# Optimization experiments

Hardware: AMD Instinct MI355X
Metric: run time of the kernel (lower is better)

## Reference

```python
import jax, jax.numpy as jnp
import numpy as np

B, N, T, D, H = 4, 8, 512, 256, 8
DK = D // H


def _dwconv(x, w, b=None):
    # x: (BN, D, T) depthwise conv, kernel 3, padding 'same', groups=D
    y = jax.lax.conv_general_dilated(
        x, w, window_strides=(1,), padding='SAME',
        feature_group_count=x.shape[1],
        dimension_numbers=('NCH', 'OIH', 'NCH'))
    if b is not None:
        y = y + b[None, :, None]
    return y


def setup_inputs() -> dict:
    key = jax.random.key(0)
    ks = jax.random.split(key, 16)
    s = 1.0 / np.sqrt(D)
    s3 = 1.0 / np.sqrt(3 * D)
    inp = {
        'query': jax.random.normal(ks[0], (B, N, T, D), jnp.float32),
        'key': jax.random.normal(ks[1], (B, N, T, D), jnp.float32),
        'value': jax.random.normal(ks[2], (B, N, T, D), jnp.float32),
        'key_padding_mask': jax.random.randint(ks[3], (B, N, T), 0, 2, jnp.int32),
        # depthwise conv params
        'w_pos': jax.random.uniform(ks[4], (D, 1, 3), jnp.float32, -0.577, 0.577),
        'b_pos': jax.random.uniform(ks[5], (D,), jnp.float32, -0.577, 0.577),
        # physics-initialized differential operators (still learnable floats)
        'w_vel': jnp.tile(jnp.array([-1.0, 0.0, 1.0], jnp.float32)[None, None, :], (D, 1, 1)),
        'w_acc': jnp.tile(jnp.array([1.0, -2.0, 1.0], jnp.float32)[None, None, :], (D, 1, 1)),
        # fusion / projection linears (stored as (in, out))
        'Wq': jax.random.uniform(ks[6], (3 * D, D), jnp.float32, -s3, s3),
        'bq': jax.random.uniform(ks[7], (D,), jnp.float32, -s3, s3),
        'Wk': jax.random.uniform(ks[8], (3 * D, D), jnp.float32, -s3, s3),
        'bk': jax.random.uniform(ks[9], (D,), jnp.float32, -s3, s3),
        'Wv': jax.random.uniform(ks[10], (D, D), jnp.float32, -s, s),
        'bv': jax.random.uniform(ks[11], (D,), jnp.float32, -s, s),
        'Wo': jax.random.uniform(ks[12], (D, D), jnp.float32, -s, s),
        'bo': jax.random.uniform(ks[13], (D,), jnp.float32, -s, s),
    }
    return inp


def reference(query, key, value, key_padding_mask,
              w_pos, b_pos, w_vel, w_acc,
              Wq, bq, Wk, bk, Wv, bv, Wo, bo):
    b, n, t, d = query.shape
    scale = jnp.float32(1.0 / np.sqrt(DK))

    def kin_feats(x):
        xin = x.reshape(b * n, t, d).transpose(0, 2, 1)  # (BN, D, T)
        p = _dwconv(xin, w_pos, b_pos)
        v = _dwconv(xin, w_vel)
        a = _dwconv(xin, w_acc)
        return jnp.concatenate([p, v, a], axis=1).transpose(0, 2, 1)  # (BN, T, 3D)

    qc = kin_feats(query)
    kc = kin_feats(key)

    Q = (qc @ Wq + bq).reshape(b, n, t, H, DK).transpose(0, 1, 3, 2, 4)  # (B,N,H,Tq,dk)
    K = (kc @ Wk + bk).reshape(b, n, t, H, DK).transpose(0, 1, 3, 2, 4)
    V = (value @ Wv + bv).reshape(b, n, t, H, DK).transpose(0, 1, 3, 2, 4)

    scores = jnp.einsum('bnhqd,bnhkd->bnhqk', Q, K) * scale
    mask = key_padding_mask.astype(bool)[:, :, None, None, :]  # (B,N,1,1,Tk)
    scores = jnp.where(mask, jnp.float32(-1e9), scores)
    attn = jax.nn.softmax(scores, axis=-1)  # dropout is identity in eval

    ctx = jnp.einsum('bnhqk,bnhkd->bnhqd', attn, V)
    ctx = ctx.transpose(0, 1, 3, 2, 4).reshape(b, n, t, d)
    return ctx @ Wo + bo
```

## Files before the change

kernel.cpp:

```cpp
#include <hip/hip_runtime.h>
#include <math.h>


typedef __attribute__((ext_vector_type(8))) short bf16x8;
typedef __attribute__((ext_vector_type(4))) float f32x4;
typedef __attribute__((ext_vector_type(4))) int i32x4;

__device__ __forceinline__ unsigned short f2bf(float f) {
    unsigned u = __float_as_uint(f);
    return (unsigned short)((u + 0x7fff + ((u >> 16) & 1)) >> 16);
}
__device__ __forceinline__ float bf2f(unsigned short h) {
    return __uint_as_float(((unsigned)h) << 16);
}
__device__ __forceinline__ float ex2(float x) {
    float r; asm("v_exp_f32 %0, %1" : "=v"(r) : "v"(x)); return r;
}
__device__ __forceinline__ int cvtpk(float lo, float hi) {
    int r; asm("v_cvt_pk_bf16_f32 %0, %1, %2" : "=v"(r) : "v"(lo), "v"(hi)); return r;
}
__device__ __forceinline__ void gll16(const void* gsrc, const void* ldst) {
    __builtin_amdgcn_global_load_lds(
        (const __attribute__((address_space(1))) unsigned int*)gsrc,
        (__attribute__((address_space(3))) unsigned int*)ldst, 16, 0, 0);
}

#define SCL (0.17677669529663689f * 1.4426950408889634f)

#define OFF_XPQ  0u
#define OFF_XPK  8421376u
#define OFF_VB   16842752u
#define OFF_BTQ  25231360u
#define OFF_BTK  25624576u
#define OFF_BEFF 26017792u
#define OFF_WVT  26019840u
#define OFF_WOT  26150912u
#define OFF_QB   26413056u
#define OFF_KB   34801664u
#define OFF_VV   43190272u
#define OFF_CTX  51578880u

__global__ __launch_bounds__(256) void cvtprep(
    const float* __restrict__ q, const float* __restrict__ k, const float* __restrict__ v,
    unsigned short* __restrict__ xpq, unsigned short* __restrict__ xpk,
    unsigned short* __restrict__ vb,
    const float* __restrict__ Wq, const float* __restrict__ Wk,
    const float* __restrict__ bq, const float* __restrict__ bk,
    const float* __restrict__ wp, const float* __restrict__ wv,
    const float* __restrict__ wa, const float* __restrict__ b_pos,
    const float* __restrict__ Wv, const float* __restrict__ Wo,
    unsigned short* __restrict__ BtQ, unsigned short* __restrict__ BtK,
    float* __restrict__ beff, unsigned short* __restrict__ WVT,
    unsigned short* __restrict__ WOT)
{
    int bid = blockIdx.x;
    if (bid < 4112) {
        int idx = bid * 256 + threadIdx.x;
        int which = idx / 526336;
        int r = idx - which * 526336;
        int bn = r / 16448;
        int rr = r - bn * 16448;
        int p = rr >> 5;
        int c8 = (rr & 31) * 8;
        const float* src = which ? k : q;
        unsigned short* dst = which ? xpk : xpq;
        unsigned o[4] = {0, 0, 0, 0};
        if (p != 0 && p != 513) {
            const float* s = src + ((size_t)(bn * 512 + p - 1) * 256 + c8);
            float4 a = *(const float4*)s;
            float4 b = *(const float4*)(s + 4);
            o[0] = f2bf(a.x) | ((unsigned)f2bf(a.y) << 16);
            o[1] = f2bf(a.z) | ((unsigned)f2bf(a.w) << 16);
            o[2] = f2bf(b.x) | ((unsigned)f2bf(b.y) << 16);
            o[3] = f2bf(b.z) | ((unsigned)f2bf(b.w) << 16);
        }
        unsigned* d = (unsigned*)(dst + ((size_t)(bn * 514 + p) * 256 + c8));
        d[0] = o[0]; d[1] = o[1]; d[2] = o[2]; d[3] = o[3];
    } else if (bid < 6160) {
        int idx = (bid - 4112) * 256 + threadIdx.x;
        int row = idx >> 5;
        int c8 = (idx & 31) * 8;
        const float* s = v + ((size_t)row * 256 + c8);
        float4 a = *(const float4*)s;
        float4 b = *(const float4*)(s + 4);
        unsigned* d = (unsigned*)(vb + ((size_t)row * 256 + c8));
        d[0] = f2bf(a.x) | ((unsigned)f2bf(a.y) << 16);
        d[1] = f2bf(a.z) | ((unsigned)f2bf(a.w) << 16);
        d[2] = f2bf(b.x) | ((unsigned)f2bf(b.y) << 16);
        d[3] = f2bf(b.z) | ((unsigned)f2bf(b.w) << 16);
    } else if (bid < 7696) {
        int idx = (bid - 6160) * 256 + threadIdx.x;
        int which = idx / 196608;
        int r = idx - which * 196608;
        int j = r >> 16;
        int rem = r & 65535;
        int n = rem >> 8;
        int d = rem & 255;
        const float* W = which ? Wk : Wq;
        float val = wp[d * 3 + j] * W[d * 256 + n]
                  + wv[d * 3 + j] * W[(256 + d) * 256 + n]
                  + wa[d * 3 + j] * W[(512 + d) * 256 + n];
        if (!which) val *= SCL;
        (which ? BtK : BtQ)[n * 768 + j * 256 + d] = f2bf(val);
    } else if (bid < 8208) {
        int idx = (bid - 7696) * 256 + threadIdx.x;
        int which = idx >> 16;
        int r = idx & 65535;
        int n = r >> 8, kk = r & 255;
        if (!which) {
            WVT[n * 256 + kk] = f2bf(Wv[kk * 256 + n]);
        } else {
            float vv = Wo[kk * 256 + n];
            unsigned short hi = f2bf(vv);
            WOT[n * 512 + kk] = hi;
            WOT[n * 512 + 256 + kk] = f2bf(vv - bf2f(hi));
        }
    } else {
        int which = bid - 8208;
        int n = threadIdx.x;
        const float* W = which ? Wk : Wq;
        const float* bb = which ? bk : bq;
        float s = bb[n];
        for (int d = 0; d < 256; ++d) s = fmaf(b_pos[d], W[d * 256 + n], s);
        if (!which) s *= SCL;
        beff[which * 256 + n] = s;
    }
}

template<typename OutT>
__device__ __forceinline__ void gemm_body(
    const unsigned short* __restrict__ A, const unsigned short* __restrict__ Bt,
    const float* __restrict__ bias, OutT* __restrict__ Out,
    int ktot, int btstride, int im2col,
    unsigned short* As, unsigned short* Bs)
{
    const int tid = threadIdx.x;
    const int wid = tid >> 6, l = tid & 63;
    const int g = l >> 4, r15 = l & 15;
    const int wm = wid & 1, wn = wid >> 1;
    const int m0 = blockIdx.x * 64, n0 = blockIdx.y * 128;

    f32x4 acc[2][4] = {};

    auto stage = [&](int k0, int b) {
        unsigned short* as = As + b * 4096;
        unsigned short* bs = Bs + b * 8192;
        #pragma unroll
        for (int qq = 0; qq < 2; ++qq) {
            int cidx = qq * 256 + wid * 64 + l;
            int row = cidx >> 3, csrc = ((cidx & 7) ^ (row & 7)) * 8;
            const unsigned short* src;
            if (im2col) {
                int seq = m0 >> 9, t0 = m0 & 511, j = k0 >> 8, c0 = k0 & 255;
                src = A + ((size_t)(seq * 514 + t0 + row + j) * 256 + c0 + csrc);
            } else {
                src = A + ((size_t)(m0 + row) * 256 + (k0 & 255) + csrc);
            }
            gll16(src, as + qq * 2048 + wid * 512);
        }
        #pragma unroll
        for (int qq = 0; qq < 4; ++qq) {
            int cidx = qq * 256 + wid * 64 + l;
            int row = cidx >> 3, csrc = ((cidx & 7) ^ (row & 7)) * 8;
            gll16(Bt + ((size_t)(n0 + row) * btstride + k0 + csrc), bs + qq * 2048 + wid * 512);
        }
    };

    stage(0, 0);
    __syncthreads();
    int b = 0;
    for (int k0 = 0; k0 < ktot; k0 += 64, b ^= 1) {
        if (k0 + 64 < ktot) stage(k0 + 64, b ^ 1);
        const unsigned short* as = As + b * 4096;
        const unsigned short* bs = Bs + b * 8192;
        #pragma unroll
        for (int s = 0; s < 2; ++s) {
            const int ch = ((s * 4 + g) ^ (r15 & 7)) * 8;
            bf16x8 af[2], bf[4];
            #pragma unroll
            for (int mt = 0; mt < 2; ++mt)
                af[mt] = *(const bf16x8*)&as[(wm * 32 + mt * 16 + r15) * 64 + ch];
            #pragma unroll
            for (int nt = 0; nt < 4; ++nt)
                bf[nt] = *(const bf16x8*)&bs[(wn * 64 + nt * 16 + r15) * 64 + ch];
            #pragma unroll
            for (int mt = 0; mt < 2; ++mt)
                #pragma unroll
                for (int nt = 0; nt < 4; ++nt)
                    acc[mt][nt] = __builtin_amdgcn_mfma_f32_16x16x32_bf16(af[mt], bf[nt], acc[mt][nt], 0, 0, 0);
        }
        __syncthreads();
    }

    #pragma unroll
    for (int nt = 0; nt < 4; ++nt) {
        const int col = n0 + wn * 64 + nt * 16 + r15;
        const float bb = bias[col];
        #pragma unroll
        for (int mt = 0; mt < 2; ++mt)
            #pragma unroll
            for (int r = 0; r < 4; ++r) {
                const size_t row = m0 + wm * 32 + mt * 16 + 4 * g + r;
                float vv = acc[mt][nt][r] + bb;
                if constexpr (sizeof(OutT) == 2) Out[row * 256 + col] = (OutT)f2bf(vv);
                else Out[row * 256 + col] = (OutT)vv;
            }
    }
}

__global__ __launch_bounds__(256) void proj_fused(
    const unsigned short* __restrict__ XPQ, const unsigned short* __restrict__ XPK,
    const unsigned short* __restrict__ VB,
    const unsigned short* __restrict__ BTQ, const unsigned short* __restrict__ BTK,
    const unsigned short* __restrict__ WVT,
    const float* __restrict__ BEFF, const float* __restrict__ bv,
    unsigned short* __restrict__ QB, unsigned short* __restrict__ KB,
    unsigned short* __restrict__ VV)
{
    __shared__ alignas(16) unsigned short As[2 * 4096];
    __shared__ alignas(16) unsigned short Bs[2 * 8192];
    const int z = blockIdx.z;
    const unsigned short* A  = z == 0 ? XPQ : (z == 1 ? XPK : VB);
    const unsigned short* Bt = z == 0 ? BTQ : (z == 1 ? BTK : WVT);
    const float* bias        = z == 0 ? BEFF : (z == 1 ? BEFF + 256 : bv);
    unsigned short* Out      = z == 0 ? QB : (z == 1 ? KB : VV);
    const int ktot = z < 2 ? 768 : 256;
    gemm_body<unsigned short>(A, Bt, bias, Out, ktot, ktot, z < 2 ? 1 : 0, As, Bs);
}

__global__ __launch_bounds__(256) void outproj(
    const unsigned short* __restrict__ CTX, const unsigned short* __restrict__ WOT,
    const float* __restrict__ bo, float* __restrict__ Out)
{
    __shared__ alignas(16) unsigned short As[2 * 4096];
    __shared__ alignas(16) unsigned short Bs[2 * 8192];
    gemm_body<float>(CTX, WOT, bo, Out, 512, 512, 0, As, Bs);
}

__global__ __launch_bounds__(256) void attn_mfma(const unsigned short* __restrict__ Qb,
                                                 const unsigned short* __restrict__ Kb,
                                                 const unsigned short* __restrict__ Vv,
                                                 const int* __restrict__ mask,
                                                 unsigned short* __restrict__ ctx) {
    __shared__ alignas(16) unsigned short Qs[64 * 32];
    __shared__ alignas(16) unsigned short Ks[2][128 * 32];
    __shared__ alignas(16) unsigned short VsT[2][32 * 136];
    __shared__ float Mb[2][128];

    const int qt = blockIdx.x, bnh = blockIdx.y;
    const int bn = bnh >> 3, h = bnh & 7;
    const int tid = threadIdx.x, wid = tid >> 6, l = tid & 63;
    const int g = l >> 4, r15 = l & 15;
    const unsigned short* Qg = Qb + (size_t)bn * 512 * 256 + h * 32;
    const unsigned short* Kg = Kb + (size_t)bn * 512 * 256 + h * 32;
    const unsigned short* Vg = Vv + (size_t)bn * 512 * 256 + h * 32;
    const int* mp = mask + bn * 512;

    auto stageK = [&](int k0, int b) {
        #pragma unroll
        for (int qq = 0; qq < 2; ++qq) {
            int cidx = qq * 256 + wid * 64 + l;
            int row = cidx >> 2, csrc = ((cidx & 3) ^ (row & 3)) * 8;
            gll16(Kg + ((size_t)(k0 + row)) * 256 + csrc, &Ks[b][qq * 2048 + wid * 512]);
        }
    };

    {
        int cidx = wid * 64 + l;
        gll16(Qg + ((size_t)(qt * 64 + (cidx >> 2))) * 256 + (cidx & 3) * 8, Qs + wid * 512);
    }
    stageK(0, 0);
    {
        #pragma unroll
        for (int qq = 0; qq < 2; ++qq) {
            int key = l + 64 * qq;
            i32x4 vr = *(const i32x4*)(const void*)(Vg + (size_t)key * 256 + wid * 8);
            #pragma unroll
            for (int i = 0; i < 4; ++i) {
                unsigned u = (unsigned)vr[i];
                VsT[0][(wid * 8 + 2 * i) * 136 + key] = (unsigned short)(u & 0xffff);
                VsT[0][(wid * 8 + 2 * i + 1) * 136 + key] = (unsigned short)(u >> 16);
            }
        }
        if (tid < 128) Mb[0][tid] = (mp[tid] != 0) ? -1e9f : 0.f;
    }
    __syncthreads();

    const bf16x8 bq = *(const bf16x8*)&Qs[(wid * 16 + r15) * 32 + g * 8];

    float mrun = -1e30f, lrun = 0.f;
    f32x4 accO[2] = {};

    for (int kt = 0; kt < 4; ++kt) {
        const int cur = kt & 1, nxt = cur ^ 1;
        const int k0n = kt * 128 + 128;

        i32x4 vr[2];
        int mraw = 0;
        if (kt < 3) {
            stageK(k0n, nxt);
            #pragma unroll
            for (int qq = 0; qq < 2; ++qq)
                vr[qq] = *(const i32x4*)(const void*)(Vg + ((size_t)(k0n + l + 64 * qq)) * 256 + wid * 8);
            if (tid < 128) mraw = mp[k0n + tid];
        }

        float p[8][4];
        float rmax = -3e38f;
        __builtin_amdgcn_s_setprio(1);
        #pragma unroll
        for (int t2 = 0; t2 < 8; ++t2) {
            const int base = 32 * (t2 >> 1) + 4 * (t2 & 1);
            const int arow = base + 8 * (r15 >> 2) + (r15 & 3);
            bf16x8 ak = *(const bf16x8*)&Ks[cur][arow * 32 + ((g ^ (arow & 3)) * 8)];
            f32x4 cin = *(const f32x4*)&Mb[cur][base + 8 * g];
            f32x4 st = __builtin_amdgcn_mfma_f32_16x16x32_bf16(ak, bq, cin, 0, 0, 0);
            #pragma unroll
            for (int r = 0; r < 4; ++r) p[t2][r] = st[r];
            rmax = fmaxf(rmax, fmaxf(fmaxf(st[0], st[1]), fmaxf(st[2], st[3])));
        }
        __builtin_amdgcn_s_setprio(0);
        rmax = fmaxf(rmax, __shfl_xor(rmax, 16, 64));
        rmax = fmaxf(rmax, __shfl_xor(rmax, 32, 64));

        if (__ballot(rmax > mrun)) {
            float mnew = fmaxf(mrun, rmax);
            float fs = ex2(mrun - mnew);
            lrun *= fs;
            accO[0] *= fs;
            accO[1] *= fs;
            mrun = mnew;
        }
        float psum = 0.f;
        #pragma unroll
        for (int t2 = 0; t2 < 8; ++t2)
            #pragma unroll
            for (int r = 0; r < 4; ++r) {
                float e = ex2(p[t2][r] - mrun);
                p[t2][r] = e;
                psum += e;
            }
        psum += __shfl_xor(psum, 16, 64);
        psum += __shfl_xor(psum, 32, 64);
        lrun += psum;

        bf16x8 pb[4];
        #pragma unroll
        for (int s = 0; s < 4; ++s) {
            i32x4 bi = {cvtpk(p[2 * s][0], p[2 * s][1]), cvtpk(p[2 * s][2], p[2 * s][3]),
                        cvtpk(p[2 * s + 1][0], p[2 * s + 1][1]), cvtpk(p[2 * s + 1][2], p[2 * s + 1][3])};
            pb[s] = __builtin_bit_cast(bf16x8, bi);
        }

        __builtin_amdgcn_s_setprio(1);
        #pragma unroll
        for (int mt = 0; mt < 2; ++mt)
            #pragma unroll
            for (int s = 0; s < 4; ++s) {
                bf16x8 av = *(const bf16x8*)&VsT[cur][(mt * 16 + r15) * 136 + 32 * s + 8 * g];
                accO[mt] = __builtin_amdgcn_mfma_f32_16x16x32_bf16(av, pb[s], accO[mt], 0, 0, 0);
            }
        __builtin_amdgcn_s_setprio(0);

        if (kt < 3) {
            #pragma unroll
            for (int qq = 0; qq < 2; ++qq) {
                int key = l + 64 * qq;
                #pragma unroll
                for (int i = 0; i < 4; ++i) {
                    unsigned u = (unsigned)vr[qq][i];
                    VsT[nxt][(wid * 8 + 2 * i) * 136 + key] = (unsigned short)(u & 0xffff);
                    VsT[nxt][(wid * 8 + 2 * i + 1) * 136 + key] = (unsigned short)(u >> 16);
                }
            }
            if (tid < 128) Mb[nxt][tid] = (mraw != 0) ? -1e9f : 0.f;
        }
        __syncthreads();
    }

    const float inv = 1.f / lrun;
    const size_t orow = (size_t)bn * 512 + qt * 64 + wid * 16 + r15;
    #pragma unroll
    for (int mt = 0; mt < 2; ++mt) {
        ushort4 o;
        o.x = f2bf(accO[mt][0] * inv);
        o.y = f2bf(accO[mt][1] * inv);
        o.z = f2bf(accO[mt][2] * inv);
        o.w = f2bf(accO[mt][3] * inv);
        *(ushort4*)&ctx[orow * 256 + h * 32 + mt * 16 + 4 * g] = o;
    }
}

extern "C" void kernel_launch(void* const* d_in, const int* in_sizes, int n_in,
                              void* d_out, int out_size, void* d_ws, size_t ws_size,
                              hipStream_t stream) {
    const float* query = (const float*)d_in[0];
    const float* key   = (const float*)d_in[1];
    const float* value = (const float*)d_in[2];
    const int*   kpm   = (const int*)d_in[3];
    const float* w_pos = (const float*)d_in[4];
    const float* b_pos = (const float*)d_in[5];
    const float* w_vel = (const float*)d_in[6];
    const float* w_acc = (const float*)d_in[7];
    const float* Wq    = (const float*)d_in[8];
    const float* bq    = (const float*)d_in[9];
    const float* Wk    = (const float*)d_in[10];
    const float* bk    = (const float*)d_in[11];
    const float* Wv    = (const float*)d_in[12];
    const float* bv    = (const float*)d_in[13];
    const float* Wo    = (const float*)d_in[14];
    const float* bo    = (const float*)d_in[15];

    unsigned char* w = (unsigned char*)d_ws;
    unsigned short* XPQ = (unsigned short*)(w + OFF_XPQ);
    unsigned short* XPK = (unsigned short*)(w + OFF_XPK);
    unsigned short* VB  = (unsigned short*)(w + OFF_VB);
    unsigned short* BTQ = (unsigned short*)(w + OFF_BTQ);
    unsigned short* BTK = (unsigned short*)(w + OFF_BTK);
    float*          BEFF= (float*)(w + OFF_BEFF);
    unsigned short* WVT = (unsigned short*)(w + OFF_WVT);
    unsigned short* WOT = (unsigned short*)(w + OFF_WOT);
    unsigned short* QB  = (unsigned short*)(w + OFF_QB);
    unsigned short* KB  = (unsigned short*)(w + OFF_KB);
    unsigned short* VV  = (unsigned short*)(w + OFF_VV);
    unsigned short* CTX = (unsigned short*)(w + OFF_CTX);

    cvtprep<<<8210, 256, 0, stream>>>(query, key, value, XPQ, XPK, VB,
                                      Wq, Wk, bq, bk, w_pos, w_vel, w_acc, b_pos,
                                      Wv, Wo, BTQ, BTK, BEFF, WVT, WOT);

    proj_fused<<<dim3(256, 2, 3), 256, 0, stream>>>(XPQ, XPK, VB, BTQ, BTK, WVT,
                                                    BEFF, bv, QB, KB, VV);

    attn_mfma<<<dim3(8, 256), 256, 0, stream>>>(QB, KB, VV, kpm, CTX);

    outproj<<<dim3(256, 2), 256, 0, stream>>>(CTX, WOT, bo, (float*)d_out);
}
```

Measured before the change: 96.66 us.

## Fuse fp32-to-bf16 input conversion into projection GEMM and use 32x32 MFMA tiles

Removes the separate pass that converted query/key/value to padded bf16 buffers. The projection GEMM now loads fp32 activations directly, handles the conv boundary padding with a validity check, and converts to bf16 in registers before writing to shared memory. The GEMM body also moves from 16x16x32 to 32x32x16 MFMA, with each block covering the full 256-wide N dimension, which halves the grid but doubles the B tile in LDS. The intent is to cut a full read and write of the activations through global memory. The cost is larger LDS use, which can lower occupancy, and fewer blocks.

```diff
diff --git a/kernel.cpp b/kernel.cpp
--- a/kernel.cpp
+++ b/kernel.cpp
@@ -4,6 +4,7 @@
 
 typedef __attribute__((ext_vector_type(8))) short bf16x8;
 typedef __attribute__((ext_vector_type(4))) float f32x4;
+typedef __attribute__((ext_vector_type(16))) float f32x16;
 typedef __attribute__((ext_vector_type(4))) int i32x4;
 
 __device__ __forceinline__ unsigned short f2bf(float f) {
@@ -27,9 +28,6 @@
 
 #define SCL (0.17677669529663689f * 1.4426950408889634f)
 
-#define OFF_XPQ  0u
-#define OFF_XPK  8421376u
-#define OFF_VB   16842752u
 #define OFF_BTQ  25231360u
 #define OFF_BTK  25624576u
 #define OFF_BEFF 26017792u
@@ -40,56 +38,24 @@
 #define OFF_VV   43190272u
 #define OFF_CTX  51578880u
 
-__global__ __launch_bounds__(256) void cvtprep(
-    const float* __restrict__ q, const float* __restrict__ k, const float* __restrict__ v,
-    unsigned short* __restrict__ xpq, unsigned short* __restrict__ xpk,
-    unsigned short* __restrict__ vb,
-    const float* __restrict__ Wq, const float* __restrict__ Wk,
-    const float* __restrict__ bq, const float* __restrict__ bk,
-    const float* __restrict__ wp, const float* __restrict__ wv,
-    const float* __restrict__ wa, const float* __restrict__ b_pos,
-    const float* __restrict__ Wv, const float* __restrict__ Wo,
-    unsigned short* __restrict__ BtQ, unsigned short* __restrict__ BtK,
-    float* __restrict__ beff, unsigned short* __restrict__ WVT,
-    unsigned short* __restrict__ WOT)
-{
+__global__ __launch_bounds__(256) void prep(const float* __restrict__ Wq,
+                                            const float* __restrict__ Wk,
+                                            const float* __restrict__ bq,
+                                            const float* __restrict__ bk,
+                                            const float* __restrict__ wp,
+                                            const float* __restrict__ wv,
+                                            const float* __restrict__ wa,
+                                            const float* __restrict__ b_pos,
+                                            const float* __restrict__ Wv,
+                                            const float* __restrict__ Wo,
+                                            unsigned short* __restrict__ BtQ,
+                                            unsigned short* __restrict__ BtK,
+                                            float* __restrict__ beff,
+                                            unsigned short* __restrict__ WVT,
+                                            unsigned short* __restrict__ WOT) {
     int bid = blockIdx.x;
-    if (bid < 4112) {
+    if (bid < 1536) {
         int idx = bid * 256 + threadIdx.x;
-        int which = idx / 526336;
-        int r = idx - which * 526336;
-        int bn = r / 16448;
-        int rr = r - bn * 16448;
-        int p = rr >> 5;
-        int c8 = (rr & 31) * 8;
-        const float* src = which ? k : q;
-        unsigned short* dst = which ? xpk : xpq;
-        unsigned o[4] = {0, 0, 0, 0};
-        if (p != 0 && p != 513) {
-            const float* s = src + ((size_t)(bn * 512 + p - 1) * 256 + c8);
-            float4 a = *(const float4*)s;
-            float4 b = *(const float4*)(s + 4);
-            o[0] = f2bf(a.x) | ((unsigned)f2bf(a.y) << 16);
-            o[1] = f2bf(a.z) | ((unsigned)f2bf(a.w) << 16);
-            o[2] = f2bf(b.x) | ((unsigned)f2bf(b.y) << 16);
-            o[3] = f2bf(b.z) | ((unsigned)f2bf(b.w) << 16);
-        }
-        unsigned* d = (unsigned*)(dst + ((size_t)(bn * 514 + p) * 256 + c8));
-        d[0] = o[0]; d[1] = o[1]; d[2] = o[2]; d[3] = o[3];
-    } else if (bid < 6160) {
-        int idx = (bid - 4112) * 256 + threadIdx.x;
-        int row = idx >> 5;
-        int c8 = (idx & 31) * 8;
-        const float* s = v + ((size_t)row * 256 + c8);
-        float4 a = *(const float4*)s;
-        float4 b = *(const float4*)(s + 4);
-        unsigned* d = (unsigned*)(vb + ((size_t)row * 256 + c8));
-        d[0] = f2bf(a.x) | ((unsigned)f2bf(a.y) << 16);
-        d[1] = f2bf(a.z) | ((unsigned)f2bf(a.w) << 16);
-        d[2] = f2bf(b.x) | ((unsigned)f2bf(b.y) << 16);
-        d[3] = f2bf(b.z) | ((unsigned)f2bf(b.w) << 16);
-    } else if (bid < 7696) {
-        int idx = (bid - 6160) * 256 + threadIdx.x;
         int which = idx / 196608;
         int r = idx - which * 196608;
         int j = r >> 16;
@@ -102,21 +68,21 @@
                   + wa[d * 3 + j] * W[(512 + d) * 256 + n];
         if (!which) val *= SCL;
         (which ? BtK : BtQ)[n * 768 + j * 256 + d] = f2bf(val);
-    } else if (bid < 8208) {
-        int idx = (bid - 7696) * 256 + threadIdx.x;
+    } else if (bid < 2048) {
+        int idx = (bid - 1536) * 256 + threadIdx.x;
         int which = idx >> 16;
         int r = idx & 65535;
-        int n = r >> 8, kk = r & 255;
+        int n = r >> 8, k = r & 255;
         if (!which) {
-            WVT[n * 256 + kk] = f2bf(Wv[kk * 256 + n]);
+            WVT[n * 256 + k] = f2bf(Wv[k * 256 + n]);
         } else {
-            float vv = Wo[kk * 256 + n];
-            unsigned short hi = f2bf(vv);
-            WOT[n * 512 + kk] = hi;
-            WOT[n * 512 + 256 + kk] = f2bf(vv - bf2f(hi));
+            float v = Wo[k * 256 + n];
+            unsigned short hi = f2bf(v);
+            WOT[n * 512 + k] = hi;
+            WOT[n * 512 + 256 + k] = f2bf(v - bf2f(hi));
         }
     } else {
-        int which = bid - 8208;
+        int which = bid - 2048;
         int n = threadIdx.x;
         const float* W = which ? Wk : Wq;
         const float* bb = which ? bk : bq;
@@ -127,90 +93,124 @@
     }
 }
 
-template<typename OutT>
-__device__ __forceinline__ void gemm_body(
-    const unsigned short* __restrict__ A, const unsigned short* __restrict__ Bt,
+template<int MODE, int KTOT, typename OutT>
+__device__ __forceinline__ void gemm32_body(
+    const void* Asrc, const unsigned short* __restrict__ Bt,
     const float* __restrict__ bias, OutT* __restrict__ Out,
-    int ktot, int btstride, int im2col,
     unsigned short* As, unsigned short* Bs)
 {
     const int tid = threadIdx.x;
     const int wid = tid >> 6, l = tid & 63;
-    const int g = l >> 4, r15 = l & 15;
-    const int wm = wid & 1, wn = wid >> 1;
-    const int m0 = blockIdx.x * 64, n0 = blockIdx.y * 128;
-
-    f32x4 acc[2][4] = {};
-
-    auto stage = [&](int k0, int b) {
-        unsigned short* as = As + b * 4096;
-        unsigned short* bs = Bs + b * 8192;
-        #pragma unroll
-        for (int qq = 0; qq < 2; ++qq) {
-            int cidx = qq * 256 + wid * 64 + l;
-            int row = cidx >> 3, csrc = ((cidx & 7) ^ (row & 7)) * 8;
-            const unsigned short* src;
-            if (im2col) {
-                int seq = m0 >> 9, t0 = m0 & 511, j = k0 >> 8, c0 = k0 & 255;
-                src = A + ((size_t)(seq * 514 + t0 + row + j) * 256 + c0 + csrc);
+    const int l31 = l & 31, h2 = l >> 5;
+    const int m0 = blockIdx.x * 64;
+    const int arow = tid >> 2, aq = tid & 3;
+
+    f32x16 acc[2][2] = {};
+    f32x4 ar[4];
+
+    auto issueB = [&](int k0, int b) {
+        #pragma unroll
+        for (int rr = 0; rr < 8; ++rr) {
+            int row = rr * 32 + (tid >> 3);
+            int srcc = ((tid & 7) ^ (row & 7)) * 8;
+            gll16(Bt + (size_t)row * KTOT + k0 + srcc,
+                  Bs + b * 16384 + (rr * 256 + wid * 64) * 8);
+        }
+    };
+    auto issueA = [&](int k0, int b) {
+        if constexpr (MODE == 0) {
+            const unsigned short* A = (const unsigned short*)Asrc;
+            #pragma unroll
+            for (int rr = 0; rr < 2; ++rr) {
+                int row = rr * 32 + (tid >> 3);
+                int srcc = ((tid & 7) ^ (row & 7)) * 8;
+                gll16(A + (size_t)(m0 + row) * 256 + (k0 & 255) + srcc,
+                      As + b * 4096 + (rr * 256 + wid * 64) * 8);
+            }
+        } else {
+            const float* X = (const float*)Asrc;
+            bool valid = true;
+            size_t off;
+            if constexpr (MODE == 1) {
+                int seq = m0 >> 9, t0 = m0 & 511;
+                int st = t0 + arow + (k0 >> 8) - 1;
+                valid = (st >= 0) && (st < 512);
+                off = (size_t)(seq * 512 + st) * 256 + (k0 & 255) + aq * 16;
             } else {
-                src = A + ((size_t)(m0 + row) * 256 + (k0 & 255) + csrc);
-            }
-            gll16(src, as + qq * 2048 + wid * 512);
-        }
-        #pragma unroll
-        for (int qq = 0; qq < 4; ++qq) {
-            int cidx = qq * 256 + wid * 64 + l;
-            int row = cidx >> 3, csrc = ((cidx & 7) ^ (row & 7)) * 8;
-            gll16(Bt + ((size_t)(n0 + row) * btstride + k0 + csrc), bs + qq * 2048 + wid * 512);
+                off = (size_t)(m0 + arow) * 256 + k0 + aq * 16;
+            }
+            #pragma unroll
+            for (int i = 0; i < 4; ++i)
+                ar[i] = valid ? *(const f32x4*)(X + off + i * 4) : (f32x4){0.f, 0.f, 0.f, 0.f};
         }
     };
-
-    stage(0, 0);
+    auto commitA = [&](int b) {
+        if constexpr (MODE != 0) {
+            i32x4 w0 = {cvtpk(ar[0][0], ar[0][1]), cvtpk(ar[0][2], ar[0][3]),
+                        cvtpk(ar[1][0], ar[1][1]), cvtpk(ar[1][2], ar[1][3])};
+            i32x4 w1 = {cvtpk(ar[2][0], ar[2][1]), cvtpk(ar[2][2], ar[2][3]),
+                        cvtpk(ar[3][0], ar[3][1]), cvtpk(ar[3][2], ar[3][3])};
+            int c0 = ((aq * 2) ^ (arow & 7)) * 8;
+            int c1 = ((aq * 2 + 1) ^ (arow & 7)) * 8;
+            *(i32x4*)&As[b * 4096 + arow * 64 + c0] = w0;
+            *(i32x4*)&As[b * 4096 + arow * 64 + c1] = w1;
+        }
+    };
+
+    issueA(0, 0);
+    issueB(0, 0);
+    commitA(0);
     __syncthreads();
+
     int b = 0;
-    for (int k0 = 0; k0 < ktot; k0 += 64, b ^= 1) {
-        if (k0 + 64 < ktot) stage(k0 + 64, b ^ 1);
+    for (int k0 = 0; k0 < KTOT; k0 += 64, b ^= 1) {
+        const bool more = (k0 + 64) < KTOT;
+        if (more) { issueA(k0 + 64, b ^ 1); issueB(k0 + 64, b ^ 1); }
         const unsigned short* as = As + b * 4096;
-        const unsigned short* bs = Bs + b * 8192;
-        #pragma unroll
-        for (int s = 0; s < 2; ++s) {
-            const int ch = ((s * 4 + g) ^ (r15 & 7)) * 8;
-            bf16x8 af[2], bf[4];
-            #pragma unroll
-            for (int mt = 0; mt < 2; ++mt)
-                af[mt] = *(const bf16x8*)&as[(wm * 32 + mt * 16 + r15) * 64 + ch];
-            #pragma unroll
-            for (int nt = 0; nt < 4; ++nt)
-                bf[nt] = *(const bf16x8*)&bs[(wn * 64 + nt * 16 + r15) * 64 + ch];
+        const unsigned short* bs = Bs + b * 16384;
+        #pragma unroll
+        for (int ks = 0; ks < 4; ++ks) {
+            bf16x8 af[2], bfr[2];
+            #pragma unroll
+            for (int mt = 0; mt < 2; ++mt) {
+                int r = mt * 32 + l31;
+                af[mt] = *(const bf16x8*)&as[r * 64 + (((ks * 2 + h2) ^ (r & 7)) * 8)];
+            }
+            #pragma unroll
+            for (int nt = 0; nt < 2; ++nt) {
+                int r = wid * 64 + nt * 32 + l31;
+                bfr[nt] = *(const bf16x8*)&bs[r * 64 + (((ks * 2 + h2) ^ (r & 7)) * 8)];
+            }
             #pragma unroll
             for (int mt = 0; mt < 2; ++mt)
                 #pragma unroll
-                for (int nt = 0; nt < 4; ++nt)
-                    acc[mt][nt] = __builtin_amdgcn_mfma_f32_16x16x32_bf16(af[mt], bf[nt], acc[mt][nt], 0, 0, 0);
-        }
+                for (int nt = 0; nt < 2; ++nt)
+                    acc[mt][nt] = __builtin_amdgcn_mfma_f32_32x32x16_bf16(af[mt], bfr[nt], acc[mt][nt], 0, 0, 0);
+        }
+        if (more) commitA(b ^ 1);
         __syncthreads();
     }
 
     #pragma unroll
-    for (int nt = 0; nt < 4; ++nt) {
-        const int col = n0 + wn * 64 + nt * 16 + r15;
+    for (int nt = 0; nt < 2; ++nt) {
+        const int col = wid * 64 + nt * 32 + l31;
         const float bb = bias[col];
         #pragma unroll
-        for (int mt = 0; mt < 2; ++mt)
-            #pragma unroll
-            for (int r = 0; r < 4; ++r) {
-                const size_t row = m0 + wm * 32 + mt * 16 + 4 * g + r;
-                float vv = acc[mt][nt][r] + bb;
-                if constexpr (sizeof(OutT) == 2) Out[row * 256 + col] = (OutT)f2bf(vv);
-                else Out[row * 256 + col] = (OutT)vv;
-            }
+        for (int mt = 0; mt < 2; ++mt) {
+            #pragma unroll
+            for (int r = 0; r < 16; ++r) {
+                const int row = m0 + mt * 32 + 4 * h2 + (r & 3) + 8 * (r >> 2);
+                float v = acc[mt][nt][r] + bb;
+                if constexpr (sizeof(OutT) == 2) Out[(size_t)row * 256 + col] = (OutT)f2bf(v);
+                else Out[(size_t)row * 256 + col] = v;
+            }
+        }
     }
 }
 
 __global__ __launch_bounds__(256) void proj_fused(
-    const unsigned short* __restrict__ XPQ, const unsigned short* __restrict__ XPK,
-    const unsigned short* __restrict__ VB,
+    const float* __restrict__ query, const float* __restrict__ key,
+    const float* __restrict__ value,
     const unsigned short* __restrict__ BTQ, const unsigned short* __restrict__ BTK,
     const unsigned short* __restrict__ WVT,
     const float* __restrict__ BEFF, const float* __restrict__ bv,
@@ -218,14 +218,11 @@
     unsigned short* __restrict__ VV)
 {
     __shared__ alignas(16) unsigned short As[2 * 4096];
-    __shared__ alignas(16) unsigned short Bs[2 * 8192];
+    __shared__ alignas(16) unsigned short Bs[2 * 16384];
     const int z = blockIdx.z;
-    const unsigned short* A  = z == 0 ? XPQ : (z == 1 ? XPK : VB);
-    const unsigned short* Bt = z == 0 ? BTQ : (z == 1 ? BTK : WVT);
-    const float* bias        = z == 0 ? BEFF : (z == 1 ? BEFF + 256 : bv);
-    unsigned short* Out      = z == 0 ? QB : (z == 1 ? KB : VV);
-    const int ktot = z < 2 ? 768 : 256;
-    gemm_body<unsigned short>(A, Bt, bias, Out, ktot, ktot, z < 2 ? 1 : 0, As, Bs);
+    if (z == 0)      gemm32_body<1, 768, unsigned short>(query, BTQ, BEFF, QB, As, Bs);
+    else if (z == 1) gemm32_body<1, 768, unsigned short>(key, BTK, BEFF + 256, KB, As, Bs);
+    else             gemm32_body<2, 256, unsigned short>(value, WVT, bv, VV, As, Bs);
 }
 
 __global__ __launch_bounds__(256) void outproj(
@@ -233,8 +230,8 @@
     const float* __restrict__ bo, float* __restrict__ Out)
 {
     __shared__ alignas(16) unsigned short As[2 * 4096];
-    __shared__ alignas(16) unsigned short Bs[2 * 8192];
-    gemm_body<float>(CTX, WOT, bo, Out, 512, 512, 0, As, Bs);
+    __shared__ alignas(16) unsigned short Bs[2 * 16384];
+    gemm32_body<0, 512, float>(CTX, WOT, bo, Out, As, Bs);
 }
 
 __global__ __launch_bounds__(256) void attn_mfma(const unsigned short* __restrict__ Qb,
@@ -412,9 +409,6 @@
     const float* bo    = (const float*)d_in[15];
 
     unsigned char* w = (unsigned char*)d_ws;
-    unsigned short* XPQ = (unsigned short*)(w + OFF_XPQ);
-    unsigned short* XPK = (unsigned short*)(w + OFF_XPK);
-    unsigned short* VB  = (unsigned short*)(w + OFF_VB);
     unsigned short* BTQ = (unsigned short*)(w + OFF_BTQ);
     unsigned short* BTK = (unsigned short*)(w + OFF_BTK);
     float*          BEFF= (float*)(w + OFF_BEFF);
@@ -425,14 +419,13 @@
     unsigned short* VV  = (unsigned short*)(w + OFF_VV);
     unsigned short* CTX = (unsigned short*)(w + OFF_CTX);
 
-    cvtprep<<<8210, 256, 0, stream>>>(query, key, value, XPQ, XPK, VB,
-                                      Wq, Wk, bq, bk, w_pos, w_vel, w_acc, b_pos,
-                                      Wv, Wo, BTQ, BTK, BEFF, WVT, WOT);
-
-    proj_fused<<<dim3(256, 2, 3), 256, 0, stream>>>(XPQ, XPK, VB, BTQ, BTK, WVT,
+    prep<<<2050, 256, 0, stream>>>(Wq, Wk, bq, bk, w_pos, w_vel, w_acc, b_pos,
+                                   Wv, Wo, BTQ, BTK, BEFF, WVT, WOT);
+
+    proj_fused<<<dim3(256, 1, 3), 256, 0, stream>>>(query, key, value, BTQ, BTK, WVT,
                                                     BEFF, bv, QB, KB, VV);
 
     attn_mfma<<<dim3(8, 256), 256, 0, stream>>>(QB, KB, VV, kpm, CTX);
 
-    outproj<<<dim3(256, 2), 256, 0, stream>>>(CTX, WOT, bo, (float*)d_out);
-}
+    outproj<<<256, 256, 0, stream>>>(CTX, WOT, bo, (float*)d_out);
+}
```

Result: no change. 95.17 us (-1.5%).

## Rewrite projection GEMMs with 128x128 tiles and 32x32x16 MFMA

Applied to the files above, without the earlier changes.

Replaces the 64x128 double-buffered GEMM body with a templated 128x128 single-buffered version that issues 32x32x16 bf16 MFMAs and takes K and the im2col mode as compile-time parameters. Grids for the projection and output GEMMs are halved to match. The larger tile raises arithmetic intensity and the bigger MFMA cuts LDS fragment reads, but dropping double buffering exposes load latency, and fewer blocks (768 and 256) reduce occupancy across the CUs.

```diff
diff --git a/kernel.cpp b/kernel.cpp
--- a/kernel.cpp
+++ b/kernel.cpp
@@ -4,6 +4,7 @@
 
 typedef __attribute__((ext_vector_type(8))) short bf16x8;
 typedef __attribute__((ext_vector_type(4))) float f32x4;
+typedef __attribute__((ext_vector_type(16))) float f32x16;
 typedef __attribute__((ext_vector_type(4))) int i32x4;
 
 __device__ __forceinline__ unsigned short f2bf(float f) {
@@ -127,84 +128,73 @@
     }
 }
 
-template<typename OutT>
-__device__ __forceinline__ void gemm_body(
+template<int KTOT, bool IM2COL, typename OutT>
+__device__ __forceinline__ void gemm97(
     const unsigned short* __restrict__ A, const unsigned short* __restrict__ Bt,
     const float* __restrict__ bias, OutT* __restrict__ Out,
-    int ktot, int btstride, int im2col,
     unsigned short* As, unsigned short* Bs)
 {
     const int tid = threadIdx.x;
     const int wid = tid >> 6, l = tid & 63;
-    const int g = l >> 4, r15 = l & 15;
-    const int wm = wid & 1, wn = wid >> 1;
-    const int m0 = blockIdx.x * 64, n0 = blockIdx.y * 128;
-
-    f32x4 acc[2][4] = {};
-
-    auto stage = [&](int k0, int b) {
-        unsigned short* as = As + b * 4096;
-        unsigned short* bs = Bs + b * 8192;
-        #pragma unroll
-        for (int qq = 0; qq < 2; ++qq) {
-            int cidx = qq * 256 + wid * 64 + l;
-            int row = cidx >> 3, csrc = ((cidx & 7) ^ (row & 7)) * 8;
-            const unsigned short* src;
-            if (im2col) {
-                int seq = m0 >> 9, t0 = m0 & 511, j = k0 >> 8, c0 = k0 & 255;
-                src = A + ((size_t)(seq * 514 + t0 + row + j) * 256 + c0 + csrc);
+    const int l31 = l & 31, h2 = l >> 5;
+    const int wm = wid >> 1, wn = wid & 1;
+    const int m0 = blockIdx.x * 128, n0 = blockIdx.y * 128;
+
+    f32x16 acc[2][2] = {};
+
+    for (int k0 = 0; k0 < KTOT; k0 += 64) {
+        __syncthreads();
+        #pragma unroll
+        for (int q = 0; q < 4; ++q) {
+            int cidx = q * 256 + wid * 64 + l;
+            int row = cidx >> 3;
+            int csrc = ((cidx & 7) ^ (row & 7)) * 8;
+            const unsigned short* asrc;
+            if constexpr (IM2COL) {
+                int seq = m0 >> 9, t0 = m0 & 511;
+                asrc = A + ((size_t)(seq * 514 + t0 + row + (k0 >> 8)) * 256 + (k0 & 255) + csrc);
             } else {
-                src = A + ((size_t)(m0 + row) * 256 + (k0 & 255) + csrc);
-            }
-            gll16(src, as + qq * 2048 + wid * 512);
-        }
-        #pragma unroll
-        for (int qq = 0; qq < 4; ++qq) {
-            int cidx = qq * 256 + wid * 64 + l;
-            int row = cidx >> 3, csrc = ((cidx & 7) ^ (row & 7)) * 8;
-            gll16(Bt + ((size_t)(n0 + row) * btstride + k0 + csrc), bs + qq * 2048 + wid * 512);
-        }
-    };
-
-    stage(0, 0);
-    __syncthreads();
-    int b = 0;
-    for (int k0 = 0; k0 < ktot; k0 += 64, b ^= 1) {
-        if (k0 + 64 < ktot) stage(k0 + 64, b ^ 1);
-        const unsigned short* as = As + b * 4096;
-        const unsigned short* bs = Bs + b * 8192;
-        #pragma unroll
-        for (int s = 0; s < 2; ++s) {
-            const int ch = ((s * 4 + g) ^ (r15 & 7)) * 8;
-            bf16x8 af[2], bf[4];
-            #pragma unroll
-            for (int mt = 0; mt < 2; ++mt)
-                af[mt] = *(const bf16x8*)&as[(wm * 32 + mt * 16 + r15) * 64 + ch];
-            #pragma unroll
-            for (int nt = 0; nt < 4; ++nt)
-                bf[nt] = *(const bf16x8*)&bs[(wn * 64 + nt * 16 + r15) * 64 + ch];
+                asrc = A + ((size_t)(m0 + row) * 256 + (k0 & 255) + csrc);
+            }
+            gll16(asrc, As + (q * 256 + wid * 64) * 8);
+            gll16(Bt + (size_t)(n0 + row) * KTOT + k0 + csrc, Bs + (q * 256 + wid * 64) * 8);
+        }
+        __syncthreads();
+        #pragma unroll
+        for (int ks = 0; ks < 4; ++ks) {
+            bf16x8 af[2], bfr[2];
+            #pragma unroll
+            for (int mt = 0; mt < 2; ++mt) {
+                int r = wm * 64 + mt * 32 + l31;
+                af[mt] = *(const bf16x8*)&As[r * 64 + (((ks * 2 + h2) ^ (r & 7)) * 8)];
+            }
+            #pragma unroll
+            for (int nt = 0; nt < 2; ++nt) {
+                int rn = wn * 64 + nt * 32 + l31;
+                bfr[nt] = *(const bf16x8*)&Bs[rn * 64 + (((ks * 2 + h2) ^ (rn & 7)) * 8)];
+            }
             #pragma unroll
             for (int mt = 0; mt < 2; ++mt)
                 #pragma unroll
-                for (int nt = 0; nt < 4; ++nt)
-                    acc[mt][nt] = __builtin_amdgcn_mfma_f32_16x16x32_bf16(af[mt], bf[nt], acc[mt][nt], 0, 0, 0);
-        }
-        __syncthreads();
+                for (int nt = 0; nt < 2; ++nt)
+                    acc[mt][nt] = __builtin_amdgcn_mfma_f32_32x32x16_bf16(af[mt], bfr[nt], acc[mt][nt], 0, 0, 0);
+        }
     }
 
     #pragma unroll
-    for (int nt = 0; nt < 4; ++nt) {
-        const int col = n0 + wn * 64 + nt * 16 + r15;
+    for (int nt = 0; nt < 2; ++nt) {
+        const int col = n0 + wn * 64 + nt * 32 + l31;
         const float bb = bias[col];
         #pragma unroll
-        for (int mt = 0; mt < 2; ++mt)
-            #pragma unroll
-            for (int r = 0; r < 4; ++r) {
-                const size_t row = m0 + wm * 32 + mt * 16 + 4 * g + r;
-                float vv = acc[mt][nt][r] + bb;
-                if constexpr (sizeof(OutT) == 2) Out[row * 256 + col] = (OutT)f2bf(vv);
-                else Out[row * 256 + col] = (OutT)vv;
-            }
+        for (int mt = 0; mt < 2; ++mt) {
+            #pragma unroll
+            for (int r = 0; r < 16; ++r) {
+                const int row = m0 + wm * 64 + mt * 32 + 4 * h2 + (r & 3) + 8 * (r >> 2);
+                float v = acc[mt][nt][r] + bb;
+                if constexpr (sizeof(OutT) == 2) Out[(size_t)row * 256 + col] = (OutT)f2bf(v);
+                else Out[(size_t)row * 256 + col] = v;
+            }
+        }
     }
 }
 
@@ -217,24 +207,21 @@
     unsigned short* __restrict__ QB, unsigned short* __restrict__ KB,
     unsigned short* __restrict__ VV)
 {
-    __shared__ alignas(16) unsigned short As[2 * 4096];
-    __shared__ alignas(16) unsigned short Bs[2 * 8192];
+    __shared__ alignas(16) unsigned short As[8192];
+    __shared__ alignas(16) unsigned short Bs[8192];
     const int z = blockIdx.z;
-    const unsigned short* A  = z == 0 ? XPQ : (z == 1 ? XPK : VB);
-    const unsigned short* Bt = z == 0 ? BTQ : (z == 1 ? BTK : WVT);
-    const float* bias        = z == 0 ? BEFF : (z == 1 ? BEFF + 256 : bv);
-    unsigned short* Out      = z == 0 ? QB : (z == 1 ? KB : VV);
-    const int ktot = z < 2 ? 768 : 256;
-    gemm_body<unsigned short>(A, Bt, bias, Out, ktot, ktot, z < 2 ? 1 : 0, As, Bs);
+    if (z == 0)      gemm97<768, true, unsigned short>(XPQ, BTQ, BEFF, QB, As, Bs);
+    else if (z == 1) gemm97<768, true, unsigned short>(XPK, BTK, BEFF + 256, KB, As, Bs);
+    else             gemm97<256, false, unsigned short>(VB, WVT, bv, VV, As, Bs);
 }
 
 __global__ __launch_bounds__(256) void outproj(
     const unsigned short* __restrict__ CTX, const unsigned short* __restrict__ WOT,
     const float* __restrict__ bo, float* __restrict__ Out)
 {
-    __shared__ alignas(16) unsigned short As[2 * 4096];
-    __shared__ alignas(16) unsigned short Bs[2 * 8192];
-    gemm_body<float>(CTX, WOT, bo, Out, 512, 512, 0, As, Bs);
+    __shared__ alignas(16) unsigned short As[8192];
+    __shared__ alignas(16) unsigned short Bs[8192];
+    gemm97<512, false, float>(CTX, WOT, bo, Out, As, Bs);
 }
 
 __global__ __launch_bounds__(256) void attn_mfma(const unsigned short* __restrict__ Qb,
@@ -429,10 +416,10 @@
                                       Wq, Wk, bq, bk, w_pos, w_vel, w_acc, b_pos,
                                       Wv, Wo, BTQ, BTK, BEFF, WVT, WOT);
 
-    proj_fused<<<dim3(256, 2, 3), 256, 0, stream>>>(XPQ, XPK, VB, BTQ, BTK, WVT,
+    proj_fused<<<dim3(128, 2, 3), 256, 0, stream>>>(XPQ, XPK, VB, BTQ, BTK, WVT,
                                                     BEFF, bv, QB, KB, VV);
 
     attn_mfma<<<dim3(8, 256), 256, 0, stream>>>(QB, KB, VV, kpm, CTX);
 
-    outproj<<<dim3(256, 2), 256, 0, stream>>>(CTX, WOT, bo, (float*)d_out);
-}
+    outproj<<<dim3(128, 2), 256, 0, stream>>>(CTX, WOT, bo, (float*)d_out);
+}
```

Result: no change. 95.38 us (-1.3%).
